# Performance work log

Hardware: AMD Instinct MI355X
Metric: run time of the kernel (lower is better)

Reference implementation:

```python
import jax, jax.numpy as jnp
import numpy as np

N_NODES = 50000
N_EDGES = 1600000
ATOM_F = 64
FP_SIZE = 2048
N_GRAPHS = 2000


def setup_inputs() -> dict:
    key = jax.random.key(0)
    ks = jax.random.split(key, 12)
    s = 1.0 / np.sqrt(ATOM_F)
    x = jax.random.normal(ks[0], (N_NODES, ATOM_F), dtype=jnp.float32)
    H1_w = jax.random.normal(ks[1], (ATOM_F, ATOM_F), dtype=jnp.float32) * s
    H1_b = jnp.zeros((ATOM_F,), dtype=jnp.float32)
    W1_w = jax.random.normal(ks[2], (FP_SIZE, ATOM_F), dtype=jnp.float32) * s
    W1_b = jnp.zeros((FP_SIZE,), dtype=jnp.float32)
    H2_w = jax.random.normal(ks[3], (ATOM_F, ATOM_F), dtype=jnp.float32) * s
    H2_b = jnp.zeros((ATOM_F,), dtype=jnp.float32)
    W2_w = jax.random.normal(ks[4], (FP_SIZE, ATOM_F), dtype=jnp.float32) * s
    W2_b = jnp.zeros((FP_SIZE,), dtype=jnp.float32)
    edge_index = jax.random.randint(ks[5], (2, N_EDGES), 0, N_NODES, dtype=jnp.int64)
    batch = jnp.sort(jax.random.randint(ks[6], (N_NODES,), 0, N_GRAPHS, dtype=jnp.int64))
    return {
        "x": x,
        "H1_w": H1_w, "H1_b": H1_b, "W1_w": W1_w, "W1_b": W1_b,
        "H2_w": H2_w, "H2_b": H2_b, "W2_w": W2_w, "W2_b": W2_b,
        "edge_index": edge_index,
        "batch": batch,
        "num_graphs": N_GRAPHS,
    }


def reference(x, H1_w, H1_b, W1_w, W1_b, H2_w, H2_b, W2_w, W2_b,
              edge_index, batch, num_graphs):
    n = x.shape[0]
    src, dst = edge_index[0], edge_index[1]

    def loop(h, Hw, Hb, Ww, Wb):
        # sum aggregation over incoming edges; '+ h' accounts for add_self_loops
        agg = jax.ops.segment_sum(h[src], dst, num_segments=n) + h
        upd = jax.nn.sigmoid(agg @ Hw.T + Hb)          # [N, atom_features]
        fp = jax.nn.softmax(upd @ Ww.T + Wb, axis=-1)  # [N, fp_size]
        return upd, fp

    h1, fp1 = loop(x, H1_w, H1_b, W1_w, W1_b)
    _, fp2 = loop(h1, H2_w, H2_b, W2_w, W2_b)
    fingerprint = fp1 + fp2
    # pool per-node fingerprints into per-graph fingerprints
    return jax.ops.segment_sum(fingerprint, batch, num_segments=num_graphs)
```

## Files before the change

kernel.cpp:

```cpp
#include <hip/hip_runtime.h>
#include <hip/hip_bf16.h>

#define AF 64
#define NFP 2048

typedef __attribute__((ext_vector_type(8))) short bf16x8;
typedef __attribute__((ext_vector_type(4))) float f32x4;

__device__ __forceinline__ ushort f2bf(float f) {
    unsigned u = __float_as_uint(f);
    return (ushort)((u + 0x7FFF + ((u >> 16) & 1)) >> 16);
}
__device__ __forceinline__ float bf2f(ushort u) {
    return __uint_as_float((unsigned)u << 16);
}

__global__ __launch_bounds__(256) void hist_kernel(
    const int* __restrict__ keys, int* __restrict__ counts, int n)
{
    int e = blockIdx.x * 256 + threadIdx.x;
    if (e < n) atomicAdd(&counts[keys[e]], 1);
}

__global__ __launch_bounds__(256) void hist_part_kernel(
    const int* __restrict__ dst, int* __restrict__ counts,
    int n_edges, int npr, int nchunks)
{
    int r = blockIdx.x & 7;
    int c = blockIdx.x >> 3;
    int lo = r * npr, hi = lo + npr;
    int per = (n_edges + nchunks - 1) / nchunks;
    int e0 = c * per;
    int e1 = e0 + per; if (e1 > n_edges) e1 = n_edges;
    for (int e = e0 + (int)threadIdx.x; e < e1; e += 256) {
        int d = dst[e];
        if (d >= lo && d < hi) atomicAdd(&counts[d], 1);
    }
}

__global__ __launch_bounds__(1024) void scan_kernel(int* data, int n)
{
    __shared__ int wsum[16];
    __shared__ int chunk_total;
    int t = threadIdx.x, lane = t & 63, w = t >> 6;
    int running = 0;
    for (int base = 0; base < n; base += 1024) {
        int i = base + t;
        int v = (i < n) ? data[i] : 0;
        int x = v;
        #pragma unroll
        for (int off = 1; off < 64; off <<= 1) {
            int y = __shfl_up(x, off);
            if (lane >= off) x += y;
        }
        if (lane == 63) wsum[w] = x;
        __syncthreads();
        if (t == 0) {
            int s = 0;
            #pragma unroll
            for (int q = 0; q < 16; ++q) { int tmp = wsum[q]; wsum[q] = s; s += tmp; }
            chunk_total = s;
        }
        __syncthreads();
        if (i < n) data[i] = x - v + wsum[w] + running;
        running += chunk_total;
        __syncthreads();
    }
    if (t == 0) data[n] = running;
}

__global__ __launch_bounds__(256) void scatter_part_kernel(
    const int* __restrict__ src, const int* __restrict__ dst,
    int* __restrict__ cursor, int* __restrict__ esrc,
    int n_edges, int npr, int nchunks)
{
    int r = blockIdx.x & 7;
    int c = blockIdx.x >> 3;
    int lo = r * npr, hi = lo + npr;
    int per = (n_edges + nchunks - 1) / nchunks;
    int e0 = c * per;
    int e1 = e0 + per; if (e1 > n_edges) e1 = n_edges;
    for (int e = e0 + (int)threadIdx.x; e < e1; e += 256) {
        int d = dst[e];
        if (d >= lo && d < hi) {
            int pos = atomicAdd(&cursor[d], 1);
            esrc[pos] = src[e];
        }
    }
}

__global__ __launch_bounds__(256) void f2bf_kernel(
    const float* __restrict__ W, ushort* __restrict__ Wbf, int n)
{
    int i = blockIdx.x * 256 + threadIdx.x;
    if (i < n) Wbf[i] = f2bf(W[i]);
}

__global__ __launch_bounds__(256) void agg_mlp_kernel(
    const ushort* __restrict__ hbf, const int* __restrict__ offsets,
    const int* __restrict__ esrc, const float* __restrict__ Hw,
    const float* __restrict__ Hb, ushort* __restrict__ outbf, int n_nodes)
{
    __shared__ float Hw_s[AF * 65];
    __shared__ __align__(16) float part[4][8][AF];
    __shared__ float a_red[4][AF];
    __shared__ float hb_s[AF];

    int t = threadIdx.x;
    for (int idx = t; idx < AF * AF; idx += 256) {
        int j = idx >> 6, k = idx & 63;
        Hw_s[j * 65 + k] = Hw[idx];
    }
    if (t < AF) hb_s[t] = Hb[t];

    int w = t >> 6, lane = t & 63;
    int sub = lane >> 3, f8 = lane & 7;
    int i = blockIdx.x * 4 + w;

    float acc[8] = {0.f, 0.f, 0.f, 0.f, 0.f, 0.f, 0.f, 0.f};
    if (i < n_nodes) {
        int o0 = offsets[i], o1 = offsets[i + 1];
        const int* ep = esrc + o0;
        int deg = o1 - o0;
        for (int j = 0; j < deg; j += 8) {
            int jj = j + sub;
            if (jj < deg) {
                int s = ep[jj];
                bf16x8 v = *(const bf16x8*)(hbf + (size_t)s * AF + f8 * 8);
                #pragma unroll
                for (int q = 0; q < 8; ++q) acc[q] += bf2f((ushort)v[q]);
            }
        }
    }
    *(float4*)&part[w][sub][f8 * 8]     = make_float4(acc[0], acc[1], acc[2], acc[3]);
    *(float4*)&part[w][sub][f8 * 8 + 4] = make_float4(acc[4], acc[5], acc[6], acc[7]);
    __syncthreads();

    if (i < n_nodes) {
        float val = bf2f(hbf[(size_t)i * AF + lane]);
        #pragma unroll
        for (int s8 = 0; s8 < 8; ++s8) val += part[w][s8][lane];
        a_red[w][lane] = val;
    }
    __syncthreads();

    if (i < n_nodes) {
        float z = hb_s[lane];
        #pragma unroll
        for (int k = 0; k < AF; ++k)
            z = fmaf(a_red[w][k], Hw_s[lane * 65 + k], z);
        float sg = 1.f / (1.f + __expf(-z));
        outbf[(size_t)i * AF + lane] = f2bf(sg);
    }
}

__global__ __launch_bounds__(256) void denom_kernel(
    const ushort* __restrict__ updbf, const ushort* __restrict__ Wbf,
    const float* __restrict__ Wb, float* __restrict__ sden, int n_nodes)
{
    __shared__ float wb_s[NFP];
    int t = threadIdx.x, wave = t >> 6, lane = t & 63;
    int G = lane >> 4, sl = lane & 15;
    for (int i = t; i < NFP / 4; i += 256)
        *(float4*)&wb_s[i * 4] = *(const float4*)&Wb[i * 4];
    __syncthreads();

    int base = blockIdx.x * 128 + wave * 32;
    bf16x8 a00, a01, a10, a11;
    {
        const ushort* p0 = updbf + (size_t)(base + sl) * AF + G * 8;
        a00 = *(const bf16x8*)p0;
        a01 = *(const bf16x8*)(p0 + 32);
        const ushort* p1 = updbf + (size_t)(base + 16 + sl) * AF + G * 8;
        a10 = *(const bf16x8*)p1;
        a11 = *(const bf16x8*)(p1 + 32);
    }
    float s0[4] = {0.f, 0.f, 0.f, 0.f};
    float s1[4] = {0.f, 0.f, 0.f, 0.f};

    #pragma unroll 2
    for (int ct = 0; ct < 128; ++ct) {
        int col = ct * 16 + sl;
        const ushort* wp = Wbf + (size_t)col * AF + G * 8;
        bf16x8 b0 = *(const bf16x8*)wp;
        bf16x8 b1 = *(const bf16x8*)(wp + 32);
        float bias = wb_s[col];
        f32x4 d0 = {0.f, 0.f, 0.f, 0.f};
        d0 = __builtin_amdgcn_mfma_f32_16x16x32_bf16(a00, b0, d0, 0, 0, 0);
        d0 = __builtin_amdgcn_mfma_f32_16x16x32_bf16(a01, b1, d0, 0, 0, 0);
        f32x4 d1 = {0.f, 0.f, 0.f, 0.f};
        d1 = __builtin_amdgcn_mfma_f32_16x16x32_bf16(a10, b0, d1, 0, 0, 0);
        d1 = __builtin_amdgcn_mfma_f32_16x16x32_bf16(a11, b1, d1, 0, 0, 0);
        #pragma unroll
        for (int r = 0; r < 4; ++r) {
            s0[r] += __expf(d0[r] + bias);
            s1[r] += __expf(d1[r] + bias);
        }
    }
    #pragma unroll
    for (int mask = 1; mask <= 8; mask <<= 1) {
        #pragma unroll
        for (int r = 0; r < 4; ++r) {
            s0[r] += __shfl_xor(s0[r], mask);
            s1[r] += __shfl_xor(s1[r], mask);
        }
    }
    if (sl == 0) {
        #pragma unroll
        for (int r = 0; r < 4; ++r) {
            int n0 = base + G * 4 + r;
            if (n0 < n_nodes) sden[n0] = 1.f / s0[r];
            int n1 = n0 + 16;
            if (n1 < n_nodes) sden[n1] = 1.f / s1[r];
        }
    }
}

template <int ACCUM>
__global__ __launch_bounds__(512) void fp_pool_graph_kernel(
    const ushort* __restrict__ updbf, const ushort* __restrict__ Wbf,
    const float* __restrict__ Wb, const float* __restrict__ sden,
    const int* __restrict__ goff, float* __restrict__ out)
{
    __shared__ __align__(16) float facc[NFP];
    __shared__ __align__(16) float wb_s[NFP];

    int t = threadIdx.x, wave = t >> 6, lane = t & 63;
    int G = lane >> 4, sl = lane & 15;
    int c0 = wave * 256;

    *(float4*)&facc[c0 + lane * 4] = make_float4(0.f, 0.f, 0.f, 0.f);
    *(float4*)&wb_s[c0 + lane * 4] = *(const float4*)&Wb[c0 + lane * 4];

    int g = blockIdx.x;
    int gs = goff[g], ge = goff[g + 1];

    for (int i0 = gs; i0 < ge; i0 += 32) {
        bf16x8 a00, a01, a10, a11;
        {
            const ushort* p0 = updbf + (size_t)(i0 + sl) * AF + G * 8;
            a00 = *(const bf16x8*)p0;
            a01 = *(const bf16x8*)(p0 + 32);
            const ushort* p1 = updbf + (size_t)(i0 + 16 + sl) * AF + G * 8;
            a10 = *(const bf16x8*)p1;
            a11 = *(const bf16x8*)(p1 + 32);
        }
        float sc0[4], sc1[4];
        #pragma unroll
        for (int r = 0; r < 4; ++r) {
            int n0 = i0 + G * 4 + r;
            sc0[r] = (n0 < ge) ? sden[n0] : 0.f;
            int n1 = n0 + 16;
            sc1[r] = (n1 < ge) ? sden[n1] : 0.f;
        }
        #pragma unroll 2
        for (int ct = 0; ct < 16; ++ct) {
            int col = c0 + ct * 16 + sl;
            const ushort* wp = Wbf + (size_t)col * AF + G * 8;
            bf16x8 b0 = *(const bf16x8*)wp;
            bf16x8 b1 = *(const bf16x8*)(wp + 32);
            float bias = wb_s[col];
            f32x4 d0 = {0.f, 0.f, 0.f, 0.f};
            d0 = __builtin_amdgcn_mfma_f32_16x16x32_bf16(a00, b0, d0, 0, 0, 0);
            d0 = __builtin_amdgcn_mfma_f32_16x16x32_bf16(a01, b1, d0, 0, 0, 0);
            f32x4 d1 = {0.f, 0.f, 0.f, 0.f};
            d1 = __builtin_amdgcn_mfma_f32_16x16x32_bf16(a10, b0, d1, 0, 0, 0);
            d1 = __builtin_amdgcn_mfma_f32_16x16x32_bf16(a11, b1, d1, 0, 0, 0);
            float c = 0.f;
            #pragma unroll
            for (int r = 0; r < 4; ++r) {
                c += __expf(d0[r] + bias) * sc0[r];
                c += __expf(d1[r] + bias) * sc1[r];
            }
            c += __shfl_xor(c, 16);
            c += __shfl_xor(c, 32);
            if (G == 0) facc[col] += c;
        }
    }

    __syncthreads();
    float4 fa = *(float4*)&facc[t * 4];
    float* po = &out[(size_t)g * NFP];
    if (ACCUM) {
        float4 oa = *(const float4*)&po[t * 4];
        fa.x += oa.x; fa.y += oa.y; fa.z += oa.z; fa.w += oa.w;
    }
    *(float4*)&po[t * 4] = fa;
}

extern "C" void kernel_launch(void* const* d_in, const int* in_sizes, int n_in,
                              void* d_out, int out_size, void* d_ws, size_t ws_size,
                              hipStream_t stream)
{
    const float* x    = (const float*)d_in[0];
    const float* H1_w = (const float*)d_in[1];
    const float* H1_b = (const float*)d_in[2];
    const float* W1_w = (const float*)d_in[3];
    const float* W1_b = (const float*)d_in[4];
    const float* H2_w = (const float*)d_in[5];
    const float* H2_b = (const float*)d_in[6];
    const float* W2_w = (const float*)d_in[7];
    const float* W2_b = (const float*)d_in[8];
    const int*   ei   = (const int*)d_in[9];
    const int*   batch= (const int*)d_in[10];

    const int n_nodes  = in_sizes[0] / AF;
    const int n_edges  = in_sizes[9] / 2;
    const int n_graphs = out_size / NFP;
    const int npad     = ((n_nodes + 127) / 128) * 128;
    const int* src = ei;
    const int* dst = ei + n_edges;
    float* out = (float*)d_out;

    ushort* xbf     = (ushort*)d_ws;
    ushort* ubf1    = xbf  + (size_t)npad * AF;
    ushort* ubf2    = ubf1 + (size_t)npad * AF;
    ushort* Wbf1    = ubf2 + (size_t)npad * AF;
    ushort* Wbf2    = Wbf1 + (size_t)NFP * AF;
    float*  sden    = (float*)(Wbf2 + (size_t)NFP * AF);
    int*    offsets = (int*)(sden + npad);
    int*    cursor  = offsets + (n_nodes + 1);
    int*    goff    = cursor + (n_nodes + 1);
    int*    esrc    = goff + (n_graphs + 1);

    const int nb = (n_nodes + 255) / 256;
    const int mlp_blocks = (n_nodes + 3) / 4;
    const int dn_blocks  = npad / 128;
    const int wn = NFP * AF;
    const int xn = n_nodes * AF;
    const int npr = (n_nodes + 7) / 8;
    const int nchunks = 256;

    f2bf_kernel<<<(xn + 255) / 256, 256, 0, stream>>>(x, xbf, xn);
    f2bf_kernel<<<(wn + 255) / 256, 256, 0, stream>>>(W1_w, Wbf1, wn);
    f2bf_kernel<<<(wn + 255) / 256, 256, 0, stream>>>(W2_w, Wbf2, wn);
    hipMemsetAsync(ubf1 + (size_t)n_nodes * AF, 0,
                   (size_t)(npad - n_nodes) * AF * sizeof(ushort), stream);
    hipMemsetAsync(ubf2 + (size_t)n_nodes * AF, 0,
                   (size_t)(npad - n_nodes) * AF * sizeof(ushort), stream);
    hipMemsetAsync(offsets, 0, (size_t)(n_nodes + 1) * sizeof(int), stream);
    hipMemsetAsync(goff, 0, (size_t)(n_graphs + 1) * sizeof(int), stream);
    hist_part_kernel<<<nchunks * 8, 256, 0, stream>>>(dst, offsets, n_edges, npr, nchunks);
    hist_kernel<<<nb, 256, 0, stream>>>(batch, goff, n_nodes);
    scan_kernel<<<1, 1024, 0, stream>>>(offsets, n_nodes);
    scan_kernel<<<1, 1024, 0, stream>>>(goff, n_graphs);
    hipMemcpyAsync(cursor, offsets, (size_t)n_nodes * sizeof(int),
                   hipMemcpyDeviceToDevice, stream);
    scatter_part_kernel<<<nchunks * 8, 256, 0, stream>>>(src, dst, cursor, esrc,
                                                         n_edges, npr, nchunks);

    agg_mlp_kernel<<<mlp_blocks, 256, 0, stream>>>(xbf, offsets, esrc,
                                                   H1_w, H1_b, ubf1, n_nodes);
    denom_kernel<<<dn_blocks, 256, 0, stream>>>(ubf1, Wbf1, W1_b, sden, n_nodes);
    fp_pool_graph_kernel<0><<<n_graphs, 512, 0, stream>>>(ubf1, Wbf1, W1_b,
                                                          sden, goff, out);

    agg_mlp_kernel<<<mlp_blocks, 256, 0, stream>>>(ubf1, offsets, esrc,
                                                   H2_w, H2_b, ubf2, n_nodes);
    denom_kernel<<<dn_blocks, 256, 0, stream>>>(ubf2, Wbf2, W2_b, sden, n_nodes);
    fp_pool_graph_kernel<1><<<n_graphs, 512, 0, stream>>>(ubf2, Wbf2, W2_b,
                                                          sden, goff, out);
}
```

Measured before the change: 671.4 us.

## Split denom columns across waves, prefetch W tiles, pool two graphs per block

The softmax-denominator kernel now gives each block 32 nodes and spreads the 2048 output columns over its 4 waves, combining the partial sums through shared memory. This yields four times as many blocks, and the bias is read from global memory instead of being staged in LDS. Both the denom and fp_pool kernels software-prefetch the next W tile into registers before the current MFMAs. The fp_pool kernel processes two graphs per block, and each wave handles only its own columns, so the end-of-block barrier is gone. The trade-off is higher register pressure and fewer fp_pool blocks, which could reduce parallelism.

```diff
diff --git a/kernel.cpp b/kernel.cpp
--- a/kernel.cpp
+++ b/kernel.cpp
@@ -3,6 +3,7 @@
 
 #define AF 64
 #define NFP 2048
+#define GPB 2
 
 typedef __attribute__((ext_vector_type(8))) short bf16x8;
 typedef __attribute__((ext_vector_type(4))) float f32x4;
@@ -158,14 +159,13 @@
     const ushort* __restrict__ updbf, const ushort* __restrict__ Wbf,
     const float* __restrict__ Wb, float* __restrict__ sden, int n_nodes)
 {
-    __shared__ float wb_s[NFP];
+    __shared__ float red[4][32];
+
     int t = threadIdx.x, wave = t >> 6, lane = t & 63;
     int G = lane >> 4, sl = lane & 15;
-    for (int i = t; i < NFP / 4; i += 256)
-        *(float4*)&wb_s[i * 4] = *(const float4*)&Wb[i * 4];
-    __syncthreads();
-
-    int base = blockIdx.x * 128 + wave * 32;
+    int cw = wave * 512;
+    int base = blockIdx.x * 32;
+
     bf16x8 a00, a01, a10, a11;
     {
         const ushort* p0 = updbf + (size_t)(base + sl) * AF + G * 8;
@@ -178,13 +178,19 @@
     float s0[4] = {0.f, 0.f, 0.f, 0.f};
     float s1[4] = {0.f, 0.f, 0.f, 0.f};
 
-    #pragma unroll 2
-    for (int ct = 0; ct < 128; ++ct) {
-        int col = ct * 16 + sl;
-        const ushort* wp = Wbf + (size_t)col * AF + G * 8;
-        bf16x8 b0 = *(const bf16x8*)wp;
-        bf16x8 b1 = *(const bf16x8*)(wp + 32);
-        float bias = wb_s[col];
+    const ushort* wp0 = Wbf + (size_t)(cw + sl) * AF + G * 8;
+    bf16x8 nb0 = *(const bf16x8*)wp0;
+    bf16x8 nb1 = *(const bf16x8*)(wp0 + 32);
+
+    #pragma unroll 4
+    for (int ct = 0; ct < 32; ++ct) {
+        bf16x8 b0 = nb0, b1 = nb1;
+        if (ct < 31) {
+            const ushort* wp = Wbf + (size_t)(cw + (ct + 1) * 16 + sl) * AF + G * 8;
+            nb0 = *(const bf16x8*)wp;
+            nb1 = *(const bf16x8*)(wp + 32);
+        }
+        float bias = Wb[cw + ct * 16 + sl];
         f32x4 d0 = {0.f, 0.f, 0.f, 0.f};
         d0 = __builtin_amdgcn_mfma_f32_16x16x32_bf16(a00, b0, d0, 0, 0, 0);
         d0 = __builtin_amdgcn_mfma_f32_16x16x32_bf16(a01, b1, d0, 0, 0, 0);
@@ -208,11 +214,15 @@
     if (sl == 0) {
         #pragma unroll
         for (int r = 0; r < 4; ++r) {
-            int n0 = base + G * 4 + r;
-            if (n0 < n_nodes) sden[n0] = 1.f / s0[r];
-            int n1 = n0 + 16;
-            if (n1 < n_nodes) sden[n1] = 1.f / s1[r];
-        }
+            red[wave][G * 4 + r]      = s0[r];
+            red[wave][16 + G * 4 + r] = s1[r];
+        }
+    }
+    __syncthreads();
+    if (t < 32) {
+        float s = red[0][t] + red[1][t] + red[2][t] + red[3][t];
+        int n = base + t;
+        if (n < n_nodes) sden[n] = 1.f / s;
     }
 }
 
@@ -220,7 +230,7 @@
 __global__ __launch_bounds__(512) void fp_pool_graph_kernel(
     const ushort* __restrict__ updbf, const ushort* __restrict__ Wbf,
     const float* __restrict__ Wb, const float* __restrict__ sden,
-    const int* __restrict__ goff, float* __restrict__ out)
+    const int* __restrict__ goff, float* __restrict__ out, int n_graphs)
 {
     __shared__ __align__(16) float facc[NFP];
     __shared__ __align__(16) float wb_s[NFP];
@@ -229,63 +239,74 @@
     int G = lane >> 4, sl = lane & 15;
     int c0 = wave * 256;
 
-    *(float4*)&facc[c0 + lane * 4] = make_float4(0.f, 0.f, 0.f, 0.f);
     *(float4*)&wb_s[c0 + lane * 4] = *(const float4*)&Wb[c0 + lane * 4];
 
-    int g = blockIdx.x;
-    int gs = goff[g], ge = goff[g + 1];
-
-    for (int i0 = gs; i0 < ge; i0 += 32) {
-        bf16x8 a00, a01, a10, a11;
-        {
-            const ushort* p0 = updbf + (size_t)(i0 + sl) * AF + G * 8;
-            a00 = *(const bf16x8*)p0;
-            a01 = *(const bf16x8*)(p0 + 32);
-            const ushort* p1 = updbf + (size_t)(i0 + 16 + sl) * AF + G * 8;
-            a10 = *(const bf16x8*)p1;
-            a11 = *(const bf16x8*)(p1 + 32);
-        }
-        float sc0[4], sc1[4];
-        #pragma unroll
-        for (int r = 0; r < 4; ++r) {
-            int n0 = i0 + G * 4 + r;
-            sc0[r] = (n0 < ge) ? sden[n0] : 0.f;
-            int n1 = n0 + 16;
-            sc1[r] = (n1 < ge) ? sden[n1] : 0.f;
-        }
-        #pragma unroll 2
-        for (int ct = 0; ct < 16; ++ct) {
-            int col = c0 + ct * 16 + sl;
-            const ushort* wp = Wbf + (size_t)col * AF + G * 8;
-            bf16x8 b0 = *(const bf16x8*)wp;
-            bf16x8 b1 = *(const bf16x8*)(wp + 32);
-            float bias = wb_s[col];
-            f32x4 d0 = {0.f, 0.f, 0.f, 0.f};
-            d0 = __builtin_amdgcn_mfma_f32_16x16x32_bf16(a00, b0, d0, 0, 0, 0);
-            d0 = __builtin_amdgcn_mfma_f32_16x16x32_bf16(a01, b1, d0, 0, 0, 0);
-            f32x4 d1 = {0.f, 0.f, 0.f, 0.f};
-            d1 = __builtin_amdgcn_mfma_f32_16x16x32_bf16(a10, b0, d1, 0, 0, 0);
-            d1 = __builtin_amdgcn_mfma_f32_16x16x32_bf16(a11, b1, d1, 0, 0, 0);
-            float c = 0.f;
+    int g0 = blockIdx.x * GPB;
+    int g1 = g0 + GPB; if (g1 > n_graphs) g1 = n_graphs;
+
+    for (int g = g0; g < g1; ++g) {
+        *(float4*)&facc[c0 + lane * 4] = make_float4(0.f, 0.f, 0.f, 0.f);
+        int gs = goff[g], ge = goff[g + 1];
+
+        for (int i0 = gs; i0 < ge; i0 += 32) {
+            bf16x8 a00, a01, a10, a11;
+            {
+                const ushort* p0 = updbf + (size_t)(i0 + sl) * AF + G * 8;
+                a00 = *(const bf16x8*)p0;
+                a01 = *(const bf16x8*)(p0 + 32);
+                const ushort* p1 = updbf + (size_t)(i0 + 16 + sl) * AF + G * 8;
+                a10 = *(const bf16x8*)p1;
+                a11 = *(const bf16x8*)(p1 + 32);
+            }
+            float sc0[4], sc1[4];
             #pragma unroll
             for (int r = 0; r < 4; ++r) {
-                c += __expf(d0[r] + bias) * sc0[r];
-                c += __expf(d1[r] + bias) * sc1[r];
+                int n0 = i0 + G * 4 + r;
+                sc0[r] = (n0 < ge) ? sden[n0] : 0.f;
+                int n1 = n0 + 16;
+                sc1[r] = (n1 < ge) ? sden[n1] : 0.f;
             }
-            c += __shfl_xor(c, 16);
-            c += __shfl_xor(c, 32);
-            if (G == 0) facc[col] += c;
-        }
-    }
-
-    __syncthreads();
-    float4 fa = *(float4*)&facc[t * 4];
-    float* po = &out[(size_t)g * NFP];
-    if (ACCUM) {
-        float4 oa = *(const float4*)&po[t * 4];
-        fa.x += oa.x; fa.y += oa.y; fa.z += oa.z; fa.w += oa.w;
-    }
-    *(float4*)&po[t * 4] = fa;
+
+            const ushort* wp0 = Wbf + (size_t)(c0 + sl) * AF + G * 8;
+            bf16x8 nb0 = *(const bf16x8*)wp0;
+            bf16x8 nb1 = *(const bf16x8*)(wp0 + 32);
+
+            #pragma unroll
+            for (int ct = 0; ct < 16; ++ct) {
+                bf16x8 b0 = nb0, b1 = nb1;
+                if (ct < 15) {
+                    const ushort* wp = Wbf + (size_t)(c0 + (ct + 1) * 16 + sl) * AF + G * 8;
+                    nb0 = *(const bf16x8*)wp;
+                    nb1 = *(const bf16x8*)(wp + 32);
+                }
+                int col = c0 + ct * 16 + sl;
+                float bias = wb_s[col];
+                f32x4 d0 = {0.f, 0.f, 0.f, 0.f};
+                d0 = __builtin_amdgcn_mfma_f32_16x16x32_bf16(a00, b0, d0, 0, 0, 0);
+                d0 = __builtin_amdgcn_mfma_f32_16x16x32_bf16(a01, b1, d0, 0, 0, 0);
+                f32x4 d1 = {0.f, 0.f, 0.f, 0.f};
+                d1 = __builtin_amdgcn_mfma_f32_16x16x32_bf16(a10, b0, d1, 0, 0, 0);
+                d1 = __builtin_amdgcn_mfma_f32_16x16x32_bf16(a11, b1, d1, 0, 0, 0);
+                float c = 0.f;
+                #pragma unroll
+                for (int r = 0; r < 4; ++r) {
+                    c += __expf(d0[r] + bias) * sc0[r];
+                    c += __expf(d1[r] + bias) * sc1[r];
+                }
+                c += __shfl_xor(c, 16);
+                c += __shfl_xor(c, 32);
+                if (G == 0) facc[col] += c;
+            }
+        }
+
+        float4 fa = *(float4*)&facc[c0 + lane * 4];
+        float* po = &out[(size_t)g * NFP];
+        if (ACCUM) {
+            float4 oa = *(const float4*)&po[c0 + lane * 4];
+            fa.x += oa.x; fa.y += oa.y; fa.z += oa.z; fa.w += oa.w;
+        }
+        *(float4*)&po[c0 + lane * 4] = fa;
+    }
 }
 
 extern "C" void kernel_launch(void* const* d_in, const int* in_sizes, int n_in,
@@ -325,7 +346,8 @@
 
     const int nb = (n_nodes + 255) / 256;
     const int mlp_blocks = (n_nodes + 3) / 4;
-    const int dn_blocks  = npad / 128;
+    const int dn_blocks  = npad / 32;
+    const int fp_blocks  = (n_graphs + GPB - 1) / GPB;
     const int wn = NFP * AF;
     const int xn = n_nodes * AF;
     const int npr = (n_nodes + 7) / 8;
@@ -334,6 +356,8 @@
     f2bf_kernel<<<(xn + 255) / 256, 256, 0, stream>>>(x, xbf, xn);
     f2bf_kernel<<<(wn + 255) / 256, 256, 0, stream>>>(W1_w, Wbf1, wn);
     f2bf_kernel<<<(wn + 255) / 256, 256, 0, stream>>>(W2_w, Wbf2, wn);
+    hipMemsetAsync(xbf + (size_t)n_nodes * AF, 0,
+                   (size_t)(npad - n_nodes) * AF * sizeof(ushort), stream);
     hipMemsetAsync(ubf1 + (size_t)n_nodes * AF, 0,
                    (size_t)(npad - n_nodes) * AF * sizeof(ushort), stream);
     hipMemsetAsync(ubf2 + (size_t)n_nodes * AF, 0,
@@ -352,12 +376,12 @@
     agg_mlp_kernel<<<mlp_blocks, 256, 0, stream>>>(xbf, offsets, esrc,
                                                    H1_w, H1_b, ubf1, n_nodes);
     denom_kernel<<<dn_blocks, 256, 0, stream>>>(ubf1, Wbf1, W1_b, sden, n_nodes);
-    fp_pool_graph_kernel<0><<<n_graphs, 512, 0, stream>>>(ubf1, Wbf1, W1_b,
-                                                          sden, goff, out);
+    fp_pool_graph_kernel<0><<<fp_blocks, 512, 0, stream>>>(ubf1, Wbf1, W1_b,
+                                                           sden, goff, out, n_graphs);
 
     agg_mlp_kernel<<<mlp_blocks, 256, 0, stream>>>(ubf1, offsets, esrc,
                                                    H2_w, H2_b, ubf2, n_nodes);
     denom_kernel<<<dn_blocks, 256, 0, stream>>>(ubf2, Wbf2, W2_b, sden, n_nodes);
-    fp_pool_graph_kernel<1><<<n_graphs, 512, 0, stream>>>(ubf2, Wbf2, W2_b,
-                                                          sden, goff, out);
-}
+    fp_pool_graph_kernel<1><<<fp_blocks, 512, 0, stream>>>(ubf2, Wbf2, W2_b,
+                                                           sden, goff, out, n_graphs);
+}
```

Result: no change. 676.3 us (+0.7%).
